# Performance work log

Hardware: AMD Instinct MI355X
Metric: run time of the kernel (lower is better)

## Reference

```python
import jax, jax.numpy as jnp
import numpy as np

P, H_OUT, D, NX = 32, 1, 256, 16
S_A = -0.1

def layernorm(x, g, b, eps=1e-5):
    mu = jnp.mean(x, axis=-1, keepdims=True)
    var = jnp.var(x, axis=-1, keepdims=True)
    return (x - mu) * jax.lax.rsqrt(var + eps) * g + b

def setup_inputs() -> dict:
    key = jax.random.key(0)
    ks = jax.random.split(key, 16)
    B, L = 8, 2048
    y = jax.random.normal(ks[0], (B, L, P), jnp.float32)
    Win = jax.random.normal(ks[1], (P, D), jnp.float32) / np.sqrt(P)
    bin_ = jnp.zeros((D,), jnp.float32)
    ng = jnp.ones((D,), jnp.float32); nb = jnp.zeros((D,), jnp.float32)
    # A = -10*rand + s_A, with A[:,0] = s_A (fix first state of each channel)
    A = -10.0 * jax.random.uniform(ks[2], (D, NX), jnp.float32) + S_A
    A = A.at[:, 0].set(S_A)
    W_B = jax.random.normal(ks[3], (NX, D), jnp.float32)
    W_C = jax.random.normal(ks[4], (NX, D), jnp.float32)
    q_delta = jax.random.normal(ks[5], (D,), jnp.float32)
    p_delta = jax.random.normal(ks[6], (1,), jnp.float32)
    nfg = jnp.ones((D,), jnp.float32); nfb = jnp.zeros((D,), jnp.float32)
    W1 = jax.random.normal(ks[7], (D, D), jnp.float32) / np.sqrt(D)
    b1 = jnp.zeros((D,), jnp.float32)
    W2 = jax.random.normal(ks[8], (D, H_OUT * P), jnp.float32) / np.sqrt(D)
    b2 = jnp.zeros((H_OUT * P,), jnp.float32)
    return {"y": y, "Win": Win, "bin_": bin_, "ng": ng, "nb": nb, "A": A,
            "W_B": W_B, "W_C": W_C, "q_delta": q_delta, "p_delta": p_delta,
            "nfg": nfg, "nfb": nfb, "W1": W1, "b1": b1, "W2": W2, "b2": b2}

def selective_scan(u, delta, A, Bm, Cm):
    # u: (B,L,D), delta: (B,L), A: (D,NX), Bm/Cm: (B,L,NX)
    dA = jnp.exp(delta[..., None, None] * A)                      # (B,L,D,NX)
    dBu = delta[..., None, None] * Bm[:, :, None, :] * u[..., None]  # (B,L,D,NX)
    x0 = jnp.zeros((u.shape[0], u.shape[2], A.shape[1]), u.dtype)
    def step(x, inp):
        dA_t, dBu_t, C_t = inp
        x = dA_t * x + dBu_t                                      # (B,D,NX)
        y_t = jnp.einsum('bdn,bn->bd', x, C_t)
        return x, y_t
    _, ys = jax.lax.scan(step, x0, (dA.transpose(1, 0, 2, 3),
                                    dBu.transpose(1, 0, 2, 3),
                                    Cm.transpose(1, 0, 2)))
    return ys.transpose(1, 0, 2)                                  # (B,L,D)

def reference(y, Win, bin_, ng, nb, A, W_B, W_C, q_delta, p_delta,
              nfg, nfb, W1, b1, W2, b2):
    B, L, _ = y.shape
    h = y @ Win + bin_                                            # (B,L,D)
    hn = layernorm(h, ng, nb)
    delta = jax.nn.softplus(p_delta[0] + jnp.einsum('bld,d->bl', hn, q_delta))
    Bm = jnp.einsum('nd,bld->bln', W_B, hn)
    Cm = jnp.einsum('nd,bld->bln', W_C, hn)
    upd = selective_scan(hn, delta, A, Bm, Cm)
    h = h + upd
    h = layernorm(h, nfg, nfb)
    out = jax.nn.gelu(h @ W1 + b1, approximate=False) @ W2 + b2
    return out.reshape(B, L, H_OUT, P)
```

## Files before the change

### kernel.cpp

```cpp
#include <hip/hip_runtime.h>
#include <math.h>

#define D 256
#define NX 16
#define L 2048
#define NBATCH 8
#define NTOK (NBATCH * L)
#define CL 32
#define NCH (L / CL)
#define LOG2E 1.44269504088896340736f

typedef float f32x4 __attribute__((ext_vector_type(4)));
typedef short bf16x8 __attribute__((ext_vector_type(8)));

__device__ __forceinline__ unsigned short f2bf(float x) {
  unsigned u = __float_as_uint(x);
  u = u + 0x7fffu + ((u >> 16) & 1u);
  return (unsigned short)(u >> 16);
}
__device__ __forceinline__ float bf2f(unsigned short h) {
  return __uint_as_float(((unsigned)h) << 16);
}

__global__ __launch_bounds__(256) void k0_prep(const float* __restrict__ A,
                                               const float* __restrict__ WB,
                                               const float* __restrict__ WC,
                                               const float* __restrict__ Win,
                                               const float* __restrict__ W1,
                                               const float* __restrict__ W2,
                                               const float* __restrict__ nfg,
                                               const float* __restrict__ nfb,
                                               float* __restrict__ At,
                                               unsigned short* __restrict__ W1fh,
                                               unsigned short* __restrict__ W1fl,
                                               unsigned short* __restrict__ W2fh,
                                               unsigned short* __restrict__ W2fl,
                                               unsigned short* __restrict__ Winfh,
                                               unsigned short* __restrict__ Winfl,
                                               unsigned short* __restrict__ Wbcfh,
                                               unsigned short* __restrict__ Wbcfl,
                                               float* __restrict__ u1,
                                               float* __restrict__ v1) {
  int i = blockIdx.x * 256 + threadIdx.x;
  if (i < 4096) {
    int d = i >> 4, n = i & 15;
    At[n * D + d] = A[i] * LOG2E;
  } else if (i < 12288) {
    int e = i - 4096;
    int j = e & 7, l = (e >> 3) & 63, tt = e >> 9;
    int k = ((l >> 4) << 3) + j;
    int n = tt * 16 + (l & 15);
    float x = Win[k * 256 + n];
    unsigned short h = f2bf(x);
    Winfh[e] = h;
    Winfl[e] = f2bf(x - bf2f(h));
  } else if (i < 20480) {
    int e = i - 12288;
    int j = e & 7, l = (e >> 3) & 63, q = e >> 9;
    int s = q >> 1, tt = q & 1;
    int k = s * 32 + ((l >> 4) << 3) + j;
    int n = tt * 16 + (l & 15);
    float x = (n < 16) ? WB[n * 256 + k] : WC[(n - 16) * 256 + k];
    unsigned short h = f2bf(x);
    Wbcfh[e] = h;
    Wbcfl[e] = f2bf(x - bf2f(h));
  } else if (i < 86016) {
    int e = i - 20480;
    int j = e & 7, l = (e >> 3) & 63, tt = (e >> 9) & 15, s = e >> 13;
    int k = s * 32 + ((l >> 4) << 3) + j;
    int n = tt * 16 + (l & 15);
    float x = W1[k * 256 + n] * nfg[k];
    unsigned short h = f2bf(x);
    W1fh[e] = h;
    W1fl[e] = f2bf(x - bf2f(h));
  } else if (i < 94208) {
    int e = i - 86016;
    int j = e & 7, l = (e >> 3) & 63, tt = (e >> 9) & 1, s = e >> 10;
    int k = s * 32 + ((l >> 4) << 3) + j;
    int n = tt * 16 + (l & 15);
    float x = W2[k * 32 + n];
    unsigned short h = f2bf(x);
    W2fh[e] = h;
    W2fl[e] = f2bf(x - bf2f(h));
  } else if (i < 94464) {
    int c = i - 94208;
    float s = 0.f;
    for (int d = 0; d < 256; ++d) s += nfg[d] * W1[d * 256 + c];
    u1[c] = s;
  } else if (i < 94720) {
    int c = i - 94464;
    float s = 0.f;
    for (int d = 0; d < 256; ++d) s += nfb[d] * W1[d * 256 + c];
    v1[c] = s;
  }
}

__global__ __launch_bounds__(512, 4) void k1a_front_scan(
    const float* __restrict__ y, const float* __restrict__ bin_,
    const float* __restrict__ ng, const float* __restrict__ nb,
    const float* __restrict__ qd, const float* __restrict__ pd,
    const float* __restrict__ At,
    const unsigned short* __restrict__ Winfh,
    const unsigned short* __restrict__ Winfl,
    const unsigned short* __restrict__ Wbcfh,
    const unsigned short* __restrict__ Wbcfl,
    float* __restrict__ hn, float* __restrict__ delta,
    float* __restrict__ Bm, float* __restrict__ Cm,
    float* __restrict__ muv, float* __restrict__ irsv,
    float* __restrict__ EX, float* __restrict__ T) {
  __shared__ float sy[32][36];
  __shared__ float sh[32][260];
  __shared__ float sB[32][NX];
  __shared__ float sred[32][16];
  __shared__ float sdelta[32];
  __shared__ float smu[32];
  __shared__ float srstd[32];
  __shared__ __align__(16) unsigned short sChA_h[32 * 256];
  __shared__ __align__(16) unsigned short sChA_l[32 * 256];
  int t = threadIdx.x;
  int l = t & 63;
  int w = t >> 6;
  int tok0 = blockIdx.x * 32;
  if (t < 256) {
    int row = t >> 3, c4 = t & 7;
    *(float4*)&sy[row][c4 * 4] = ((const float4*)(y + (size_t)tok0 * 32))[t];
  }
  __syncthreads();
  f32x4 acc[2][2];
  {
    bf16x8 yah[2], yal[2];
    int k0 = (l >> 4) << 3;
    #pragma unroll
    for (int m = 0; m < 2; ++m) {
      int row = m * 16 + (l & 15);
      float4 f0 = *(float4*)&sy[row][k0];
      float4 f1 = *(float4*)&sy[row][k0 + 4];
      float v0 = f0.x, v1_ = f0.y, v2 = f0.z, v3 = f0.w;
      float v4 = f1.x, v5 = f1.y, v6 = f1.z, v7 = f1.w;
      unsigned short h0 = f2bf(v0), h1 = f2bf(v1_), h2 = f2bf(v2), h3 = f2bf(v3);
      unsigned short h4 = f2bf(v4), h5 = f2bf(v5), h6 = f2bf(v6), h7 = f2bf(v7);
      yah[m][0] = (short)h0; yah[m][1] = (short)h1; yah[m][2] = (short)h2; yah[m][3] = (short)h3;
      yah[m][4] = (short)h4; yah[m][5] = (short)h5; yah[m][6] = (short)h6; yah[m][7] = (short)h7;
      yal[m][0] = (short)f2bf(v0 - bf2f(h0)); yal[m][1] = (short)f2bf(v1_ - bf2f(h1));
      yal[m][2] = (short)f2bf(v2 - bf2f(h2)); yal[m][3] = (short)f2bf(v3 - bf2f(h3));
      yal[m][4] = (short)f2bf(v4 - bf2f(h4)); yal[m][5] = (short)f2bf(v5 - bf2f(h5));
      yal[m][6] = (short)f2bf(v6 - bf2f(h6)); yal[m][7] = (short)f2bf(v7 - bf2f(h7));
    }
    const bf16x8* Bh = (const bf16x8*)Winfh;
    const bf16x8* Bl = (const bf16x8*)Winfl;
    #pragma unroll
    for (int n = 0; n < 2; ++n) {
      int tt = w * 2 + n;
      bf16x8 bh = Bh[tt * 64 + l];
      bf16x8 bl = Bl[tt * 64 + l];
      #pragma unroll
      for (int m = 0; m < 2; ++m) {
        f32x4 a = {0.f, 0.f, 0.f, 0.f};
        a = __builtin_amdgcn_mfma_f32_16x16x32_bf16(yah[m], bh, a, 0, 0, 0);
        a = __builtin_amdgcn_mfma_f32_16x16x32_bf16(yal[m], bh, a, 0, 0, 0);
        a = __builtin_amdgcn_mfma_f32_16x16x32_bf16(yah[m], bl, a, 0, 0, 0);
        a = __builtin_amdgcn_mfma_f32_16x16x32_bf16(yal[m], bl, a, 0, 0, 0);
        acc[m][n] = a;
      }
    }
  }
  int c0 = w * 32 + (l & 15), c1 = c0 + 16;
  {
    float b0 = bin_[c0], b1v = bin_[c1];
    #pragma unroll
    for (int m = 0; m < 2; ++m)
      #pragma unroll
      for (int r = 0; r < 4; ++r) { acc[m][0][r] += b0; acc[m][1][r] += b1v; }
  }
  {
    #pragma unroll
    for (int m = 0; m < 2; ++m)
      #pragma unroll
      for (int r = 0; r < 4; ++r) {
        float a0 = acc[m][0][r], a1 = acc[m][1][r];
        float s1 = a0 + a1;
        float s2 = a0 * a0 + a1 * a1;
        #pragma unroll
        for (int off = 1; off < 16; off <<= 1) {
          s1 += __shfl_xor(s1, off);
          s2 += __shfl_xor(s2, off);
        }
        if ((l & 15) == 0) {
          int tok = m * 16 + ((l >> 4) << 2) + r;
          sred[tok][w * 2] = s1;
          sred[tok][w * 2 + 1] = s2;
        }
      }
  }
  __syncthreads();
  if (t < 32) {
    float s1 = 0.f, s2 = 0.f;
    #pragma unroll
    for (int q = 0; q < 8; ++q) { s1 += sred[t][q * 2]; s2 += sred[t][q * 2 + 1]; }
    float mu = s1 * (1.f / D);
    float var = s2 * (1.f / D) - mu * mu;
    float rstd = rsqrtf(var + 1e-5f);
    smu[t] = mu;
    srstd[t] = rstd;
    muv[tok0 + t] = mu;
    irsv[tok0 + t] = sqrtf(var + 1e-5f);
  }
  __syncthreads();
  {
    float g0 = ng[c0], g1 = ng[c1];
    float nb0 = nb[c0], nb1 = nb[c1];
    float q0 = qd[c0], q1 = qd[c1];
    float ddv[2][4];
    #pragma unroll
    for (int m = 0; m < 2; ++m)
      #pragma unroll
      for (int r = 0; r < 4; ++r) {
        int tok = m * 16 + ((l >> 4) << 2) + r;
        float mu = smu[tok], rstd = srstd[tok];
        float h0 = (acc[m][0][r] - mu) * rstd * g0 + nb0;
        float h1 = (acc[m][1][r] - mu) * rstd * g1 + nb1;
        sh[tok][c0] = h0;
        sh[tok][c1] = h1;
        float dx = h0 * q0 + h1 * q1;
        #pragma unroll
        for (int off = 1; off < 16; off <<= 1) dx += __shfl_xor(dx, off);
        ddv[m][r] = dx;
      }
    if ((l & 15) == 0) {
      #pragma unroll
      for (int m = 0; m < 2; ++m)
        #pragma unroll
        for (int r = 0; r < 4; ++r)
          sred[m * 16 + ((l >> 4) << 2) + r][w] = ddv[m][r];
    }
  }
  __syncthreads();
  if (t < 32) {
    float dsum = 0.f;
    #pragma unroll
    for (int q = 0; q < 8; ++q) dsum += sred[t][q];
    float xx = pd[0] + dsum;
    float dv = (xx > 20.f) ? xx : log1pf(expf(xx));
    delta[tok0 + t] = dv;
    sdelta[t] = dv;
    float tv = dv;
    #pragma unroll
    for (int off = 1; off < 32; off <<= 1) tv += __shfl_xor(tv, off);
    if (t == 0) T[blockIdx.x] = tv;
  }
  {
    int row = t & 31;
    int cq = (t >> 5) * 16;
    float4 f0 = *(float4*)&sh[row][cq];
    float4 f1 = *(float4*)&sh[row][cq + 4];
    float4 f2 = *(float4*)&sh[row][cq + 8];
    float4 f3 = *(float4*)&sh[row][cq + 12];
    float vv[16] = {f0.x, f0.y, f0.z, f0.w, f1.x, f1.y, f1.z, f1.w,
                    f2.x, f2.y, f2.z, f2.w, f3.x, f3.y, f3.z, f3.w};
    unsigned hw[8], lw[8];
    #pragma unroll
    for (int p = 0; p < 8; ++p) {
      unsigned short ha = f2bf(vv[2 * p]), hb = f2bf(vv[2 * p + 1]);
      unsigned short la = f2bf(vv[2 * p] - bf2f(ha));
      unsigned short lb = f2bf(vv[2 * p + 1] - bf2f(hb));
      hw[p] = (unsigned)ha | ((unsigned)hb << 16);
      lw[p] = (unsigned)la | ((unsigned)lb << 16);
    }
    unsigned base = (unsigned)row * 512;
    #pragma unroll
    for (int g = 0; g < 2; ++g) {
      unsigned off = ((unsigned)(cq * 2 + g * 16)) ^ ((unsigned)(row & 7) << 4);
      uint4 hv4 = {hw[g * 4], hw[g * 4 + 1], hw[g * 4 + 2], hw[g * 4 + 3]};
      uint4 lv4 = {lw[g * 4], lw[g * 4 + 1], lw[g * 4 + 2], lw[g * 4 + 3]};
      *(uint4*)((char*)sChA_h + base + off) = hv4;
      *(uint4*)((char*)sChA_l + base + off) = lv4;
    }
  }
  __syncthreads();
  if (w < 4) {
    int mw = w & 1, nw = w >> 1;
    int row = mw * 16 + (l & 15);
    unsigned abase = (unsigned)row * 512;
    const bf16x8* B2h = (const bf16x8*)Wbcfh;
    const bf16x8* B2l = (const bf16x8*)Wbcfl;
    f32x4 acc2 = {0.f, 0.f, 0.f, 0.f};
    #pragma unroll
    for (int s = 0; s < 8; ++s) {
      unsigned off = ((unsigned)(s * 64 + ((l >> 4) << 4))) ^ ((unsigned)(row & 7) << 4);
      bf16x8 ah = *(const bf16x8*)((const char*)sChA_h + abase + off);
      bf16x8 al = *(const bf16x8*)((const char*)sChA_l + abase + off);
      int bi = (s * 2 + nw) * 64 + l;
      bf16x8 bh = B2h[bi];
      bf16x8 bl = B2l[bi];
      acc2 = __builtin_amdgcn_mfma_f32_16x16x32_bf16(ah, bh, acc2, 0, 0, 0);
      acc2 = __builtin_amdgcn_mfma_f32_16x16x32_bf16(al, bh, acc2, 0, 0, 0);
      acc2 = __builtin_amdgcn_mfma_f32_16x16x32_bf16(ah, bl, acc2, 0, 0, 0);
      acc2 = __builtin_amdgcn_mfma_f32_16x16x32_bf16(al, bl, acc2, 0, 0, 0);
    }
    int tokr = mw * 16 + ((l >> 4) << 2);
    int colc = l & 15;
    if (nw == 0) {
      #pragma unroll
      for (int r = 0; r < 4; ++r) {
        Bm[(size_t)(tok0 + tokr + r) * NX + colc] = acc2[r];
        sB[tokr + r][colc] = acc2[r];
      }
    } else {
      #pragma unroll
      for (int r = 0; r < 4; ++r)
        Cm[(size_t)(tok0 + tokr + r) * NX + colc] = acc2[r];
    }
  } else {
    float4* dst = (float4*)(hn + (size_t)tok0 * D);
    for (int i = t - 256; i < 2048; i += 256) {
      int row = i >> 6, c4 = i & 63;
      dst[i] = *(float4*)&sh[row][c4 * 4];
    }
  }
  __syncthreads();
  {
    int half = t >> 8;
    int d = t & 255;
    float a8[8], x8[8];
    #pragma unroll
    for (int n = 0; n < 8; ++n) {
      a8[n] = At[(half * 8 + n) * D + d];
      x8[n] = 0.f;
    }
    for (int lo = 0; lo < CL; ++lo) {
      float dlt = sdelta[lo];
      float du = dlt * sh[lo][d];
      #pragma unroll
      for (int n = 0; n < 8; ++n)
        x8[n] = fmaf(exp2f(dlt * a8[n]), x8[n], du * sB[lo][half * 8 + n]);
    }
    size_t exbase = (size_t)blockIdx.x * (NX * D) + d;
    #pragma unroll
    for (int n = 0; n < 8; ++n) EX[exbase + (half * 8 + n) * D] = x8[n];
  }
}

__global__ __launch_bounds__(64) void k2b_chunkscan(
    const float* __restrict__ At, const float* __restrict__ T,
    float* __restrict__ EX) {
  __shared__ float sT[NCH];
  int b = blockIdx.x >> 6;
  int rem = ((blockIdx.x & 63) << 6) | threadIdx.x;
  sT[threadIdx.x] = T[b * NCH + threadIdx.x];
  __syncthreads();
  float A2 = At[rem];
  size_t base = ((size_t)b << 18) + rem;
  float eq[8];
  #pragma unroll
  for (int j = 0; j < 8; ++j) eq[j] = EX[base + ((size_t)j << 12)];
  float x = 0.f;
  #pragma unroll 8
  for (int c = 0; c < NCH; ++c) {
    float e = eq[c & 7];
    if (c + 8 < NCH) eq[c & 7] = EX[base + ((size_t)(c + 8) << 12)];
    EX[base + ((size_t)c << 12)] = x;
    x = fmaf(exp2f(sT[c] * A2), x, e);
  }
}

__device__ __forceinline__ float gelu_exact(float x) {
  return 0.5f * x * (1.f + erff(x * 0.70710678118654752440f));
}

__global__ __launch_bounds__(512, 4) void k2cd_scan_mlp(
    const float* __restrict__ hn, const float* __restrict__ delta,
    const float* __restrict__ Bm, const float* __restrict__ Cm,
    const float* __restrict__ At, const float* __restrict__ EX,
    const float* __restrict__ muv, const float* __restrict__ irsv,
    const float* __restrict__ ng, const float* __restrict__ nb,
    const unsigned short* __restrict__ W1fh, const unsigned short* __restrict__ W1fl,
    const unsigned short* __restrict__ W2fh, const unsigned short* __restrict__ W2fl,
    const float* __restrict__ u1, const float* __restrict__ v1,
    const float* __restrict__ b1, const float* __restrict__ b2,
    float* __restrict__ out) {
  __shared__ __align__(16) unsigned short sAh[32 * 256];
  __shared__ __align__(16) unsigned short sAl[32 * 256];
  __shared__ float sB[32][NX];
  __shared__ float sC[32][NX];
  __shared__ float sdelta[32];
  __shared__ float smu1[32];
  __shared__ float sirs1[32];
  __shared__ float srstd2[32];
  __shared__ float smur2[32];
  int t = threadIdx.x;
  int l = t & 63, w = t >> 6;
  int tok0 = blockIdx.x * 32;
  size_t tokbase = (size_t)tok0;
  if (t < 32) {
    sdelta[t] = delta[tokbase + t];
    smu1[t] = muv[tokbase + t];
    sirs1[t] = irsv[tokbase + t];
  }
  ((float*)sB)[t] = Bm[tokbase * NX + t];
  ((float*)sC)[t] = Cm[tokbase * NX + t];
  float a16[16], x16[16];
  float nb_d = 0.f, invg = 1.f;
  if (t < 256) {
    size_t exbase = (size_t)blockIdx.x * (NX * D) + t;
    #pragma unroll
    for (int n = 0; n < 16; ++n) {
      a16[n] = At[n * D + t];
      x16[n] = EX[exbase + n * D];
    }
    nb_d = nb[t];
    invg = 1.0f / ng[t];
  }
  __syncthreads();
  if (t < 256) {
    for (int lo = 0; lo < CL; ++lo) {
      float hv = hn[(tokbase + lo) * D + t];
      float dlt = sdelta[lo];
      float du = dlt * hv;
      float p = 0.f;
      #pragma unroll
      for (int n = 0; n < 16; ++n) {
        x16[n] = fmaf(exp2f(dlt * a16[n]), x16[n], du * sB[lo][n]);
        p = fmaf(x16[n], sC[lo][n], p);
      }
      float h = fmaf((hv - nb_d) * invg, sirs1[lo], smu1[lo]);
      float v = h + p;
      unsigned short vh = f2bf(v);
      unsigned short vl = f2bf(v - bf2f(vh));
      unsigned off16 = ((unsigned)(t * 2)) ^ ((unsigned)((lo & 7) << 4));
      *(unsigned short*)((char*)sAh + lo * 512 + off16) = vh;
      *(unsigned short*)((char*)sAl + lo * 512 + off16) = vl;
    }
  }
  __syncthreads();
  {
    #pragma unroll
    for (int p = 0; p < 4; ++p) {
      int tok = w * 4 + p;
      unsigned off = ((unsigned)(l * 8)) ^ ((unsigned)((tok & 7) << 4));
      uint2 hv2 = *(uint2*)((char*)sAh + tok * 512 + off);
      uint2 lv2 = *(uint2*)((char*)sAl + tok * 512 + off);
      float v0 = bf2f((unsigned short)(hv2.x & 0xffff)) + bf2f((unsigned short)(lv2.x & 0xffff));
      float v1_ = bf2f((unsigned short)(hv2.x >> 16)) + bf2f((unsigned short)(lv2.x >> 16));
      float v2 = bf2f((unsigned short)(hv2.y & 0xffff)) + bf2f((unsigned short)(lv2.y & 0xffff));
      float v3 = bf2f((unsigned short)(hv2.y >> 16)) + bf2f((unsigned short)(lv2.y >> 16));
      float s1 = v0 + v1_ + v2 + v3;
      float s2 = v0 * v0 + v1_ * v1_ + v2 * v2 + v3 * v3;
      #pragma unroll
      for (int off2 = 1; off2 < 64; off2 <<= 1) {
        s1 += __shfl_xor(s1, off2);
        s2 += __shfl_xor(s2, off2);
      }
      if (l == 0) {
        float mu = s1 * (1.f / D);
        float var = s2 * (1.f / D) - mu * mu;
        float rstd = rsqrtf(var + 1e-5f);
        srstd2[tok] = rstd;
        smur2[tok] = mu * rstd;
      }
    }
  }
  __syncthreads();
  const bf16x8* B1h = (const bf16x8*)W1fh;
  const bf16x8* B1l = (const bf16x8*)W1fl;
  f32x4 acc[2][2];
  #pragma unroll
  for (int m = 0; m < 2; ++m)
    #pragma unroll
    for (int n = 0; n < 2; ++n) {
      f32x4 z4 = {0.f, 0.f, 0.f, 0.f};
      acc[m][n] = z4;
    }
  #pragma unroll 2
  for (int s = 0; s < 8; ++s) {
    bf16x8 ah[2], al[2];
    #pragma unroll
    for (int m = 0; m < 2; ++m) {
      int row = m * 16 + (l & 15);
      unsigned off16 = ((unsigned)(s * 64 + ((l >> 4) << 4))) ^ ((unsigned)(row & 7) << 4);
      ah[m] = *(const bf16x8*)((const char*)sAh + row * 512 + off16);
      al[m] = *(const bf16x8*)((const char*)sAl + row * 512 + off16);
    }
    #pragma unroll
    for (int n = 0; n < 2; ++n) {
      int bi = (s * 16 + w * 2 + n) * 64 + l;
      bf16x8 bh = B1h[bi];
      bf16x8 bl = B1l[bi];
      #pragma unroll
      for (int m = 0; m < 2; ++m) {
        acc[m][n] = __builtin_amdgcn_mfma_f32_16x16x32_bf16(ah[m], bh, acc[m][n], 0, 0, 0);
        acc[m][n] = __builtin_amdgcn_mfma_f32_16x16x32_bf16(al[m], bh, acc[m][n], 0, 0, 0);
        acc[m][n] = __builtin_amdgcn_mfma_f32_16x16x32_bf16(ah[m], bl, acc[m][n], 0, 0, 0);
        acc[m][n] = __builtin_amdgcn_mfma_f32_16x16x32_bf16(al[m], bl, acc[m][n], 0, 0, 0);
      }
    }
  }
  __syncthreads();
  #pragma unroll
  for (int n = 0; n < 2; ++n) {
    int colz = w * 32 + n * 16 + (l & 15);
    float u1c = u1[colz];
    float v1c = v1[colz] + b1[colz];
    #pragma unroll
    for (int m = 0; m < 2; ++m) {
      #pragma unroll
      for (int r = 0; r < 4; ++r) {
        int row = m * 16 + ((l >> 4) << 2) + r;
        float zpre = acc[m][n][r] * srstd2[row] - smur2[row] * u1c + v1c;
        float zv = gelu_exact(zpre);
        unsigned short zh = f2bf(zv);
        unsigned short zl = f2bf(zv - bf2f(zh));
        unsigned off16 = ((unsigned)(colz * 2)) ^ ((unsigned)(row & 7) << 4);
        *(unsigned short*)((char*)sAh + row * 512 + off16) = zh;
        *(unsigned short*)((char*)sAl + row * 512 + off16) = zl;
      }
    }
  }
  __syncthreads();
  if (w < 4) {
    int mw = w >> 1, nw = w & 1;
    const bf16x8* B2h = (const bf16x8*)W2fh;
    const bf16x8* B2l = (const bf16x8*)W2fl;
    f32x4 acc2 = {0.f, 0.f, 0.f, 0.f};
    #pragma unroll 2
    for (int s = 0; s < 8; ++s) {
      int row = mw * 16 + (l & 15);
      unsigned off16 = ((unsigned)(s * 64 + ((l >> 4) << 4))) ^ ((unsigned)(row & 7) << 4);
      bf16x8 zh8 = *(const bf16x8*)((const char*)sAh + row * 512 + off16);
      bf16x8 zl8 = *(const bf16x8*)((const char*)sAl + row * 512 + off16);
      int bi = (s * 2 + nw) * 64 + l;
      bf16x8 bh = B2h[bi];
      bf16x8 bl = B2l[bi];
      acc2 = __builtin_amdgcn_mfma_f32_16x16x32_bf16(zh8, bh, acc2, 0, 0, 0);
      acc2 = __builtin_amdgcn_mfma_f32_16x16x32_bf16(zl8, bh, acc2, 0, 0, 0);
      acc2 = __builtin_amdgcn_mfma_f32_16x16x32_bf16(zh8, bl, acc2, 0, 0, 0);
      acc2 = __builtin_amdgcn_mfma_f32_16x16x32_bf16(zl8, bl, acc2, 0, 0, 0);
    }
    int colo = nw * 16 + (l & 15);
    float b2v = b2[colo];
    #pragma unroll
    for (int r = 0; r < 4; ++r) {
      int row = mw * 16 + ((l >> 4) << 2) + r;
      out[(size_t)(tok0 + row) * 32 + colo] = acc2[r] + b2v;
    }
  }
}

extern "C" void kernel_launch(void* const* d_in, const int* in_sizes, int n_in,
                              void* d_out, int out_size, void* d_ws, size_t ws_size,
                              hipStream_t stream) {
  const float* y    = (const float*)d_in[0];
  const float* Win  = (const float*)d_in[1];
  const float* bin_ = (const float*)d_in[2];
  const float* ng   = (const float*)d_in[3];
  const float* nb   = (const float*)d_in[4];
  const float* A    = (const float*)d_in[5];
  const float* WB   = (const float*)d_in[6];
  const float* WC   = (const float*)d_in[7];
  const float* qd   = (const float*)d_in[8];
  const float* pd   = (const float*)d_in[9];
  const float* nfg  = (const float*)d_in[10];
  const float* nfb  = (const float*)d_in[11];
  const float* W1   = (const float*)d_in[12];
  const float* b1   = (const float*)d_in[13];
  const float* W2   = (const float*)d_in[14];
  const float* b2   = (const float*)d_in[15];

  float* ws = (float*)d_ws;
  float* hnbuf = ws;
  float* delta = ws + 4194304;
  float* Bm    = delta + NTOK;
  float* Cm    = Bm + NTOK * NX;
  float* muv   = Cm + NTOK * NX;
  float* irsv  = muv + NTOK;
  float* Tbuf  = irsv + NTOK;
  float* At    = Tbuf + NBATCH * NCH;
  float* EX    = At + D * NX;
  unsigned short* W1fh  = (unsigned short*)(EX + 2097152);
  unsigned short* W1fl  = W1fh + 65536;
  unsigned short* W2fh  = W1fl + 65536;
  unsigned short* W2fl  = W2fh + 8192;
  unsigned short* Winfh = W2fl + 8192;
  unsigned short* Winfl = Winfh + 8192;
  unsigned short* Wbcfh = Winfl + 8192;
  unsigned short* Wbcfl = Wbcfh + 8192;
  float* u1 = (float*)(Wbcfl + 8192);
  float* v1 = u1 + 256;

  k0_prep<<<370, 256, 0, stream>>>(A, WB, WC, Win, W1, W2, nfg, nfb, At,
                                   W1fh, W1fl, W2fh, W2fl,
                                   Winfh, Winfl, Wbcfh, Wbcfl, u1, v1);
  k1a_front_scan<<<NTOK / 32, 512, 0, stream>>>(y, bin_, ng, nb, qd, pd, At,
                                                Winfh, Winfl, Wbcfh, Wbcfl,
                                                hnbuf, delta, Bm, Cm,
                                                muv, irsv, EX, Tbuf);
  k2b_chunkscan<<<NBATCH * 64, 64, 0, stream>>>(At, Tbuf, EX);
  k2cd_scan_mlp<<<NTOK / 32, 512, 0, stream>>>(hnbuf, delta, Bm, Cm, At, EX,
                                               muv, irsv, ng, nb,
                                               W1fh, W1fl, W2fh, W2fl,
                                               u1, v1, b1, b2, (float*)d_out);
}
```

Baseline: 194.0 us.

## Compute intra-chunk scan output in front kernel, apply carry-in as closed-form correction

The front kernel now runs the full 16-state intra-chunk scan with zero initial state. It writes the partial output (residual plus scan contribution) and a per-token cumulative delta sum, so the later kernel no longer needs hn, delta, Bm, mu or sigma. The second kernel adds the carried-in chunk state through exp(cumdelta*A)*C, which has no sequential dependence, and splits the 32 tokens across all 512 threads. The aim is to take the serial scan off the critical path of the MLP kernel and cut workspace traffic. In exchange the front kernel does twice the state work on half its threads, and the correction recomputes exponentials per token.

```diff
diff --git a/kernel.cpp b/kernel.cpp
--- a/kernel.cpp
+++ b/kernel.cpp
@@ -104,17 +104,18 @@
     const unsigned short* __restrict__ Winfl,
     const unsigned short* __restrict__ Wbcfh,
     const unsigned short* __restrict__ Wbcfl,
-    float* __restrict__ hn, float* __restrict__ delta,
-    float* __restrict__ Bm, float* __restrict__ Cm,
-    float* __restrict__ muv, float* __restrict__ irsv,
+    float* __restrict__ vpart, float* __restrict__ cdsg,
+    float* __restrict__ Cm,
     float* __restrict__ EX, float* __restrict__ T) {
   __shared__ float sy[32][36];
   __shared__ float sh[32][260];
   __shared__ float sB[32][NX];
+  __shared__ float sC[32][NX];
   __shared__ float sred[32][16];
   __shared__ float sdelta[32];
   __shared__ float smu[32];
   __shared__ float srstd[32];
+  __shared__ float ssig[32];
   __shared__ __align__(16) unsigned short sChA_h[32 * 256];
   __shared__ __align__(16) unsigned short sChA_l[32 * 256];
   int t = threadIdx.x;
@@ -122,8 +123,8 @@
   int w = t >> 6;
   int tok0 = blockIdx.x * 32;
   if (t < 256) {
-    int row = t >> 3, c4 = t & 7;
-    *(float4*)&sy[row][c4 * 4] = ((const float4*)(y + (size_t)tok0 * 32))[t];
+    *(float4*)&sy[t >> 3][(t & 7) * 4] =
+        ((const float4*)(y + (size_t)tok0 * 32))[t];
   }
   __syncthreads();
   f32x4 acc[2][2];
@@ -202,8 +203,7 @@
     float rstd = rsqrtf(var + 1e-5f);
     smu[t] = mu;
     srstd[t] = rstd;
-    muv[tok0 + t] = mu;
-    irsv[tok0 + t] = sqrtf(var + 1e-5f);
+    ssig[t] = sqrtf(var + 1e-5f);
   }
   __syncthreads();
   {
@@ -241,12 +241,15 @@
     for (int q = 0; q < 8; ++q) dsum += sred[t][q];
     float xx = pd[0] + dsum;
     float dv = (xx > 20.f) ? xx : log1pf(expf(xx));
-    delta[tok0 + t] = dv;
     sdelta[t] = dv;
-    float tv = dv;
-    #pragma unroll
-    for (int off = 1; off < 32; off <<= 1) tv += __shfl_xor(tv, off);
-    if (t == 0) T[blockIdx.x] = tv;
+    float c = dv;
+    #pragma unroll
+    for (int off = 1; off < 32; off <<= 1) {
+      float o = __shfl_up(c, off);
+      if (t >= off) c += o;
+    }
+    cdsg[tok0 + t] = c;
+    if (t == 31) T[blockIdx.x] = c;
   }
   {
     int row = t & 31;
@@ -301,42 +304,52 @@
     int colc = l & 15;
     if (nw == 0) {
       #pragma unroll
+      for (int r = 0; r < 4; ++r) sB[tokr + r][colc] = acc2[r];
+    } else {
+      #pragma unroll
       for (int r = 0; r < 4; ++r) {
-        Bm[(size_t)(tok0 + tokr + r) * NX + colc] = acc2[r];
-        sB[tokr + r][colc] = acc2[r];
-      }
-    } else {
-      #pragma unroll
-      for (int r = 0; r < 4; ++r)
         Cm[(size_t)(tok0 + tokr + r) * NX + colc] = acc2[r];
-    }
-  } else {
-    float4* dst = (float4*)(hn + (size_t)tok0 * D);
-    for (int i = t - 256; i < 2048; i += 256) {
-      int row = i >> 6, c4 = i & 63;
-      dst[i] = *(float4*)&sh[row][c4 * 4];
-    }
-  }
-  __syncthreads();
-  {
-    int half = t >> 8;
-    int d = t & 255;
-    float a8[8], x8[8];
-    #pragma unroll
-    for (int n = 0; n < 8; ++n) {
-      a8[n] = At[(half * 8 + n) * D + d];
-      x8[n] = 0.f;
-    }
+        sC[tokr + r][colc] = acc2[r];
+      }
+    }
+  }
+  __syncthreads();
+  if (t < 256) {
+    int d = t;
+    float a16v[16], x16v[16];
+    size_t exbase = (size_t)blockIdx.x * (NX * D) + d;
+    #pragma unroll
+    for (int n = 0; n < 16; ++n) {
+      a16v[n] = At[n * D + d];
+      x16v[n] = 0.f;
+    }
+    float nb_d = nb[d];
+    float invg = 1.0f / ng[d];
+    float* vout = vpart + (size_t)tok0 * D + d;
     for (int lo = 0; lo < CL; ++lo) {
+      float hnv = sh[lo][d];
       float dlt = sdelta[lo];
-      float du = dlt * sh[lo][d];
-      #pragma unroll
-      for (int n = 0; n < 8; ++n)
-        x8[n] = fmaf(exp2f(dlt * a8[n]), x8[n], du * sB[lo][half * 8 + n]);
-    }
-    size_t exbase = (size_t)blockIdx.x * (NX * D) + d;
-    #pragma unroll
-    for (int n = 0; n < 8; ++n) EX[exbase + (half * 8 + n) * D] = x8[n];
+      float du = dlt * hnv;
+      float Bv[16], Cvv[16];
+      *(float4*)&Bv[0]  = *(float4*)&sB[lo][0];
+      *(float4*)&Bv[4]  = *(float4*)&sB[lo][4];
+      *(float4*)&Bv[8]  = *(float4*)&sB[lo][8];
+      *(float4*)&Bv[12] = *(float4*)&sB[lo][12];
+      *(float4*)&Cvv[0]  = *(float4*)&sC[lo][0];
+      *(float4*)&Cvv[4]  = *(float4*)&sC[lo][4];
+      *(float4*)&Cvv[8]  = *(float4*)&sC[lo][8];
+      *(float4*)&Cvv[12] = *(float4*)&sC[lo][12];
+      float p = 0.f;
+      #pragma unroll
+      for (int n = 0; n < 16; ++n) {
+        x16v[n] = fmaf(exp2f(dlt * a16v[n]), x16v[n], du * Bv[n]);
+        p = fmaf(x16v[n], Cvv[n], p);
+      }
+      float h = fmaf((hnv - nb_d) * invg, ssig[lo], smu[lo]);
+      vout[(size_t)lo * D] = h + p;
+    }
+    #pragma unroll
+    for (int n = 0; n < 16; ++n) EX[exbase + n * D] = x16v[n];
   }
 }
 
@@ -368,11 +381,9 @@
 }
 
 __global__ __launch_bounds__(512, 4) void k2cd_scan_mlp(
-    const float* __restrict__ hn, const float* __restrict__ delta,
-    const float* __restrict__ Bm, const float* __restrict__ Cm,
+    const float* __restrict__ vpart, const float* __restrict__ cdsg,
+    const float* __restrict__ Cm,
     const float* __restrict__ At, const float* __restrict__ EX,
-    const float* __restrict__ muv, const float* __restrict__ irsv,
-    const float* __restrict__ ng, const float* __restrict__ nb,
     const unsigned short* __restrict__ W1fh, const unsigned short* __restrict__ W1fl,
     const unsigned short* __restrict__ W2fh, const unsigned short* __restrict__ W2fl,
     const float* __restrict__ u1, const float* __restrict__ v1,
@@ -380,55 +391,39 @@
     float* __restrict__ out) {
   __shared__ __align__(16) unsigned short sAh[32 * 256];
   __shared__ __align__(16) unsigned short sAl[32 * 256];
-  __shared__ float sB[32][NX];
-  __shared__ float sC[32][NX];
-  __shared__ float sdelta[32];
-  __shared__ float smu1[32];
-  __shared__ float sirs1[32];
   __shared__ float srstd2[32];
   __shared__ float smur2[32];
   int t = threadIdx.x;
   int l = t & 63, w = t >> 6;
   int tok0 = blockIdx.x * 32;
   size_t tokbase = (size_t)tok0;
-  if (t < 32) {
-    sdelta[t] = delta[tokbase + t];
-    smu1[t] = muv[tokbase + t];
-    sirs1[t] = irsv[tokbase + t];
-  }
-  ((float*)sB)[t] = Bm[tokbase * NX + t];
-  ((float*)sC)[t] = Cm[tokbase * NX + t];
-  float a16[16], x16[16];
-  float nb_d = 0.f, invg = 1.f;
-  if (t < 256) {
-    size_t exbase = (size_t)blockIdx.x * (NX * D) + t;
+  {
+    int g = t >> 8, d = t & 255;
+    float a16v[16], xe[16];
+    size_t exbase = (size_t)blockIdx.x * (NX * D) + d;
     #pragma unroll
     for (int n = 0; n < 16; ++n) {
-      a16[n] = At[n * D + t];
-      x16[n] = EX[exbase + n * D];
-    }
-    nb_d = nb[t];
-    invg = 1.0f / ng[t];
-  }
-  __syncthreads();
-  if (t < 256) {
-    for (int lo = 0; lo < CL; ++lo) {
-      float hv = hn[(tokbase + lo) * D + t];
-      float dlt = sdelta[lo];
-      float du = dlt * hv;
-      float p = 0.f;
+      a16v[n] = At[n * D + d];
+      xe[n] = EX[exbase + n * D];
+    }
+    const float* vp_base = vpart + (tokbase + g * 16) * D + d;
+    #pragma unroll 4
+    for (int q = 0; q < 16; ++q) {
+      int tok = g * 16 + q;
+      float vp = vp_base[(size_t)q * D];
+      float ct = cdsg[tokbase + tok];
+      float pf = 0.f;
       #pragma unroll
       for (int n = 0; n < 16; ++n) {
-        x16[n] = fmaf(exp2f(dlt * a16[n]), x16[n], du * sB[lo][n]);
-        p = fmaf(x16[n], sC[lo][n], p);
-      }
-      float h = fmaf((hv - nb_d) * invg, sirs1[lo], smu1[lo]);
-      float v = h + p;
+        float cv = Cm[(tokbase + tok) * NX + n];
+        pf = fmaf(cv * exp2f(ct * a16v[n]), xe[n], pf);
+      }
+      float v = vp + pf;
       unsigned short vh = f2bf(v);
       unsigned short vl = f2bf(v - bf2f(vh));
-      unsigned off16 = ((unsigned)(t * 2)) ^ ((unsigned)((lo & 7) << 4));
-      *(unsigned short*)((char*)sAh + lo * 512 + off16) = vh;
-      *(unsigned short*)((char*)sAl + lo * 512 + off16) = vl;
+      unsigned off16 = ((unsigned)(d * 2)) ^ ((unsigned)((tok & 7) << 4));
+      *(unsigned short*)((char*)sAh + tok * 512 + off16) = vh;
+      *(unsigned short*)((char*)sAl + tok * 512 + off16) = vl;
     }
   }
   __syncthreads();
@@ -566,9 +561,9 @@
   const float* b2   = (const float*)d_in[15];
 
   float* ws = (float*)d_ws;
-  float* hnbuf = ws;
-  float* delta = ws + 4194304;
-  float* Bm    = delta + NTOK;
+  float* vpart = ws;
+  float* cdsg  = ws + 4194304;
+  float* Bm    = cdsg + NTOK;
   float* Cm    = Bm + NTOK * NX;
   float* muv   = Cm + NTOK * NX;
   float* irsv  = muv + NTOK;
@@ -591,11 +586,9 @@
                                    Winfh, Winfl, Wbcfh, Wbcfl, u1, v1);
   k1a_front_scan<<<NTOK / 32, 512, 0, stream>>>(y, bin_, ng, nb, qd, pd, At,
                                                 Winfh, Winfl, Wbcfh, Wbcfl,
-                                                hnbuf, delta, Bm, Cm,
-                                                muv, irsv, EX, Tbuf);
+                                                vpart, cdsg, Cm, EX, Tbuf);
   k2b_chunkscan<<<NBATCH * 64, 64, 0, stream>>>(At, Tbuf, EX);
-  k2cd_scan_mlp<<<NTOK / 32, 512, 0, stream>>>(hnbuf, delta, Bm, Cm, At, EX,
-                                               muv, irsv, ng, nb,
+  k2cd_scan_mlp<<<NTOK / 32, 512, 0, stream>>>(vpart, cdsg, Cm, At, EX,
                                                W1fh, W1fl, W2fh, W2fl,
                                                u1, v1, b1, b2, (float*)d_out);
 }
```

Result: no change. 194.5 us (+0.3%).
